# Kernel optimization log

Measured on AMD Instinct MI355X. Metric: run time of the kernel, lower is better.

The kernel has to match this reference:

```python
import jax, jax.numpy as jnp
import numpy as np

WIN = 7      # window_size (square)
HEADS = 6    # num_heads


def setup_inputs() -> dict:
    key = jax.random.key(0)
    k0, k1, k2, k3 = jax.random.split(key, 4)
    B, C, H, W = 8, 384, 56, 56
    x = jax.random.normal(k0, (B, C, H, W), jnp.float32)
    # 1x1 conv weights stored as (out, in) matrices
    w_qkv = jax.random.normal(k1, (3 * C, C), jnp.float32) * 0.02
    b_qkv = jnp.zeros((3 * C,), jnp.float32)
    w_proj = jax.random.normal(k2, (C, C), jnp.float32) * 0.02
    b_proj = jnp.zeros((C,), jnp.float32)
    bias_table = jax.random.normal(k3, (WIN * WIN, HEADS), jnp.float32) * 0.02
    return {"x": x, "w_qkv": w_qkv, "b_qkv": b_qkv, "w_proj": w_proj,
            "b_proj": b_proj, "bias_table": bias_table}


def reference(x, w_qkv, b_qkv, w_proj, b_proj, bias_table):
    B, C, H, W = x.shape
    heads, win = HEADS, WIN
    dph = C // heads
    scale = dph ** -0.5
    # qkv 1x1 conv -> (B, 3C, H, W)
    qkv = jnp.einsum('bcij,oc->boij', x, w_qkv) + b_qkv[None, :, None, None]
    q = qkv[:, :C] * scale
    k = qkv[:, C:2 * C]
    v = qkv[:, 2 * C:]
    p = win // 2
    kp = jnp.pad(k, ((0, 0), (0, 0), (p, p), (p, p)))  # (B,C,H+6,W+6)
    vp = jnp.pad(v, ((0, 0), (0, 0), (p, p), (p, p)))
    qh = q.reshape(B, heads, dph, H, W)
    # local window QK scores: fixed 49 shifted slices (no big patch tensor)
    scores = []
    for idx in range(win * win):
        dy, dx = idx // win, idx % win
        ks = kp[:, :, dy:dy + H, dx:dx + W].reshape(B, heads, dph, H, W)
        scores.append(jnp.einsum('bhdij,bhdij->bhij', qh, ks))
    attn = jnp.stack(scores, axis=2)  # (B, heads, 49, H, W)
    # forward() adds relative_position_bias * 0 (faithful no-op)
    attn = attn + bias_table.T.reshape(1, heads, win * win, 1, 1) * 0.0
    attn = jax.nn.softmax(attn, axis=2)
    # apply attention to V via the same 49 shifted slices
    out = jnp.zeros((B, heads, dph, H, W), x.dtype)
    for idx in range(win * win):
        dy, dx = idx // win, idx % win
        vs = vp[:, :, dy:dy + H, dx:dx + W].reshape(B, heads, dph, H, W)
        out = out + attn[:, :, idx][:, :, None] * vs
    out = out.reshape(B, C, H, W)
    # proj 1x1 conv; proj_drop has p=0.0 -> identity
    out = jnp.einsum('bcij,oc->boij', out, w_proj) + b_proj[None, :, None, None]
    return out
```

## Files before the change

kernel.cpp:

```cpp
#include <hip/hip_runtime.h>
#include <hip/hip_bf16.h>
#include <stdint.h>

#define HWsz 3136
#define Hh   56
#define Cc   384
#define NHEADS 6
#define NB   8

typedef __attribute__((ext_vector_type(8))) short short8;
typedef __attribute__((ext_vector_type(4))) short short4v;
typedef __attribute__((ext_vector_type(4))) float f32x4;

static __device__ __forceinline__ short f2bf(float f) {
  __hip_bfloat16 h = __float2bfloat16(f);
  return (short)__builtin_bit_cast(unsigned short, h);
}
static __device__ __forceinline__ void gload16(const void* g, void* l) {
  __builtin_amdgcn_global_load_lds(
      (const __attribute__((address_space(1))) void*)g,
      (__attribute__((address_space(3))) void*)l, 16, 0, 0);
}

__global__ void prep_weights(const float* __restrict__ wq, const float* __restrict__ wp,
                             short* __restrict__ wqt, short* __restrict__ wpt) {
  int stride = gridDim.x * blockDim.x;
  for (int i = blockIdx.x * blockDim.x + threadIdx.x; i < 3 * Cc * Cc; i += stride) {
    int o = i / Cc, k = i - o * Cc;
    float v = wq[i] * (o < Cc ? 0.125f : 1.0f);
    wqt[(((o >> 7) * 12 + (k >> 5)) * 128 + (o & 127)) * 40 + (k & 31)] = f2bf(v);
  }
  for (int i = blockIdx.x * blockDim.x + threadIdx.x; i < Cc * Cc; i += stride) {
    int o = i / Cc, k = i - o * Cc;
    wpt[(((o >> 7) * 12 + (k >> 5)) * 128 + (o & 127)) * 40 + (k & 31)] = f2bf(wp[i]);
  }
}

__global__ __launch_bounds__(256) void transpose_x(const float* __restrict__ x,
                                                   short* __restrict__ xTt) {
  __shared__ float tf[32][129];
  const int blk = blockIdx.x;
  const int b = blk & 7;
  const int idx = blk >> 3;
  const int pni = idx >> 2;
  const int kg  = idx & 3;
  const int p0 = pni * 128;
  const int t = threadIdx.x;
  const float* xb = x + (size_t)b * Cc * HWsz;
  short* outb = xTt + ((size_t)(b * 25 + pni)) * 12 * 5120;
  const int cc = t >> 3, pq = t & 7;
  const int orow = t >> 1, ohf = t & 1;
  for (int k0 = kg * 3; k0 < kg * 3 + 3; ++k0) {
    const float* crow = xb + (size_t)(k0 * 32 + cc) * HWsz;
#pragma unroll
    for (int i = 0; i < 4; ++i) {
      int p = p0 + pq * 16 + i * 4;
      if (p > HWsz - 4) p = HWsz - 4;
      f32x4 v = *(const f32x4*)(crow + p);
      tf[cc][pq * 16 + i * 4 + 0] = v[0];
      tf[cc][pq * 16 + i * 4 + 1] = v[1];
      tf[cc][pq * 16 + i * 4 + 2] = v[2];
      tf[cc][pq * 16 + i * 4 + 3] = v[3];
    }
    __syncthreads();
    short8 s0, s1;
#pragma unroll
    for (int i = 0; i < 8; ++i) s0[i] = f2bf(tf[ohf * 16 + i][orow]);
#pragma unroll
    for (int i = 0; i < 8; ++i) s1[i] = f2bf(tf[ohf * 16 + 8 + i][orow]);
    short* orp = outb + k0 * 5120 + orow * 40 + ohf * 16;
    *(short8*)(orp)     = s0;
    *(short8*)(orp + 8) = s1;
    __syncthreads();
  }
}

template<int MODE>
__global__ __launch_bounds__(256) void gemm_bf16(
    const short* __restrict__ At, const short* __restrict__ Bt,
    const float* __restrict__ bias, void* __restrict__ o1, void* __restrict__ o2)
{
  constexpr int NOM = (MODE == 0 ? 9 : 3);
  const int b   = blockIdx.x & 7;
  const int idx = blockIdx.x >> 3;
  const int omi = idx % NOM;
  const int pni = idx / NOM;
  const int om0 = omi * 128, pn0 = pni * 128;
  __shared__ short lA[5120];
  __shared__ short lB[5120];
  const int t = threadIdx.x, lane = t & 63, wave = t >> 6;
  const int wm = (wave >> 1) * 64, wn = (wave & 1) * 64;
  const int fr = lane & 15, fo = lane >> 4;
  f32x4 acc[4][4] = {};
  const short* Abase = At + omi * 12 * 5120;
  const short* Bbase = Bt + ((size_t)(b * 25 + pni)) * 12 * 5120;

  for (int k0i = 0; k0i < 12; ++k0i) {
    __syncthreads();
    const short* Ats = Abase + k0i * 5120;
    const short* Bts = Bbase + k0i * 5120;
#pragma unroll
    for (int c = 0; c < 5; ++c) {
      const int g = wave * 5 + c;
      const short* src = (g < 10 ? Ats + g * 512 : Bts + (g - 10) * 512) + lane * 8;
      short* dst = (g < 10 ? lA + g * 512 : lB + (g - 10) * 512);
      gload16(src, dst);
    }
    __syncthreads();
    short8 af[4], bfr[4];
#pragma unroll
    for (int m = 0; m < 4; ++m) af[m]  = *(const short8*)(lA + (wm + m * 16 + fr) * 40 + fo * 8);
#pragma unroll
    for (int n = 0; n < 4; ++n) bfr[n] = *(const short8*)(lB + (wn + n * 16 + fr) * 40 + fo * 8);
#pragma unroll
    for (int m = 0; m < 4; ++m)
#pragma unroll
      for (int n = 0; n < 4; ++n)
        acc[m][n] = __builtin_amdgcn_mfma_f32_16x16x32_bf16(af[m], bfr[n], acc[m][n], 0, 0, 0);
  }
  if (MODE == 0) {
    if (om0 < 768) {
      short* outq = (short*)o1 + (size_t)b * HWsz * 768;
#pragma unroll
      for (int m = 0; m < 4; ++m) {
        int ob = om0 + wm + m * 16 + (lane >> 4) * 4;
        float bs[4];
#pragma unroll
        for (int r = 0; r < 4; ++r) { int o = ob + r; bs[r] = bias[o] * (o < Cc ? 0.125f : 1.0f); }
#pragma unroll
        for (int n = 0; n < 4; ++n) {
          int p = pn0 + wn + n * 16 + fr;
          if (p < HWsz) {
            short4v s;
#pragma unroll
            for (int r = 0; r < 4; ++r) s[r] = f2bf(acc[m][n][r] + bs[r]);
            *(short4v*)(outq + (size_t)p * 768 + ob) = s;
          }
        }
      }
    } else {
      short* vtp = (short*)o2;
#pragma unroll
      for (int m = 0; m < 4; ++m) {
        int ob = om0 + wm + m * 16 + (lane >> 4) * 4;
#pragma unroll
        for (int n = 0; n < 4; ++n) {
          int p = pn0 + wn + n * 16 + fr;
          if (p < HWsz) {
            int ii = p / Hh, jj = p % Hh;
#pragma unroll
            for (int r = 0; r < 4; ++r) {
              int ch = ob + r - 768;
              vtp[((b * Cc + ch) * 62 + ii + 3) * 64 + jj + 3] = f2bf(acc[m][n][r] + bias[ob + r]);
            }
          }
        }
      }
    }
  } else {
    float* outo = (float*)o1 + (size_t)b * Cc * HWsz;
#pragma unroll
    for (int m = 0; m < 4; ++m) {
      int ob = om0 + wm + m * 16 + (lane >> 4) * 4;
#pragma unroll
      for (int n = 0; n < 4; ++n) {
        int p = pn0 + wn + n * 16 + fr;
        if (p < HWsz) {
#pragma unroll
          for (int r = 0; r < 4; ++r)
            outo[(size_t)(ob + r) * HWsz + p] = acc[m][n][r] + bias[ob + r];
        }
      }
    }
  }
}

__global__ __launch_bounds__(256) void attn_mfma(
    const short* __restrict__ qkv,
    const short* __restrict__ vtp,
    short* __restrict__ aoutT)
{
  __shared__ short P[64 * 40];
  const int blk = blockIdx.x;
  const int b = blk & 7;
  const int r_ = blk >> 3;
  const int h = r_ / 49;
  const int tile = r_ % 49;
  const int i0 = (tile / 7) * 8, j0 = (tile % 7) * 8;
  const int t = threadIdx.x, lane = t & 63, w = t >> 6;
  const int fr = lane & 15, fo = lane >> 4;

  const int q_idx = w * 16 + fr;
  const int qr = q_idx >> 3, qc = q_idx & 7;
  const int qkvb = b * HWsz * 768;

  const short* qp = qkv + qkvb + ((i0 + qr) * Hh + j0 + qc) * 768 + h * 64 + fo * 8;
  short8 qf0 = *(const short8*)(qp);
  short8 qf1 = *(const short8*)(qp + 32);

  const int kj = j0 + fr - 3;
  const bool jok = (unsigned)kj < (unsigned)Hh;
  const int kjs = kj < 0 ? 0 : (kj > Hh - 1 ? Hh - 1 : kj);
  const short* kcol = qkv + qkvb + Cc + h * 64 + fo * 8;

  const short8 z = (short8)0;
  f32x4 oacc[4] = {};
  float sum = 0.f;

#pragma unroll 2
  for (int kc = 0; kc < 7; ++kc) {
    short8 kf[2][2];
#pragma unroll
    for (int mloc = 0; mloc < 2; ++mloc) {
      int ki = i0 + 2 * kc + mloc - 3;
      bool ok = jok && ((unsigned)ki < (unsigned)Hh);
      int kis = ki < 0 ? 0 : (ki > Hh - 1 ? Hh - 1 : ki);
      const short8* ka = (const short8*)(kcol + (kis * Hh + kjs) * 768);
      short8 k0 = ka[0], k1 = ka[4];
      kf[mloc][0] = ok ? k0 : z;
      kf[mloc][1] = ok ? k1 : z;
    }
    short8 vf[4];
    const int vrow = i0 + 2 * kc + (fo >> 1);
    const int vcol = j0 + (fo & 1) * 8;
#pragma unroll
    for (int n = 0; n < 4; ++n)
      vf[n] = *(const short8*)(vtp + ((b * Cc + h * 64 + 16 * n + fr) * 62 + vrow) * 64 + vcol);
    f32x4 s0 = {}, s1 = {};
    s0 = __builtin_amdgcn_mfma_f32_16x16x32_bf16(kf[0][0], qf0, s0, 0, 0, 0);
    s0 = __builtin_amdgcn_mfma_f32_16x16x32_bf16(kf[0][1], qf1, s0, 0, 0, 0);
    s1 = __builtin_amdgcn_mfma_f32_16x16x32_bf16(kf[1][0], qf0, s1, 0, 0, 0);
    s1 = __builtin_amdgcn_mfma_f32_16x16x32_bf16(kf[1][1], qf1, s1, 0, 0, 0);
#pragma unroll
    for (int mloc = 0; mloc < 2; ++mloc) {
      const f32x4 sv = mloc ? s1 : s0;
      int dpr = 2 * kc + mloc - qr;
      bool rok = (unsigned)dpr <= 6u;
      short4v pk;
#pragma unroll
      for (int r = 0; r < 4; ++r) {
        int dpc = fo * 4 + r - qc;
        float e = (rok && (unsigned)dpc <= 6u) ? __expf(sv[r]) : 0.f;
        sum += e;
        pk[r] = f2bf(e);
      }
      *(short4v*)(P + q_idx * 40 + mloc * 16 + fo * 4) = pk;
    }
    short8 pa = *(const short8*)(P + q_idx * 40 + fo * 8);
#pragma unroll
    for (int n = 0; n < 4; ++n)
      oacc[n] = __builtin_amdgcn_mfma_f32_16x16x32_bf16(pa, vf[n], oacc[n], 0, 0, 0);
  }

  sum += __shfl_xor(sum, 16);
  sum += __shfl_xor(sum, 32);
  float inv[4];
#pragma unroll
  for (int r = 0; r < 4; ++r) inv[r] = 1.0f / __shfl(sum, fo * 4 + r);
  const int owr = i0 + 2 * w + (fo >> 1);
  const int owc = j0 + (fo & 1) * 4;
  short* ab = aoutT + (size_t)b * 25 * 12 * 5120;
#pragma unroll
  for (int n = 0; n < 4; ++n) {
    const int k0 = 2 * h + (n >> 1);
    const int kk = 16 * (n & 1) + fr;
#pragma unroll
    for (int r = 0; r < 4; ++r) {
      int p = owr * Hh + owc + r;
      ab[((size_t)((p >> 7) * 12 + k0)) * 5120 + (p & 127) * 40 + kk] = f2bf(oacc[n][r] * inv[r]);
    }
  }
}

extern "C" void kernel_launch(void* const* d_in, const int* in_sizes, int n_in,
                              void* d_out, int out_size, void* d_ws, size_t ws_size,
                              hipStream_t stream) {
  const float* x      = (const float*)d_in[0];
  const float* w_qkv  = (const float*)d_in[1];
  const float* b_qkv  = (const float*)d_in[2];
  const float* w_proj = (const float*)d_in[3];
  const float* b_proj = (const float*)d_in[4];

  char* ws = (char*)d_ws;
  short* qk  = (short*)ws;
  short* vtp = (short*)(ws + 38535168);
  short* xTt = (short*)(ws + 38535168 + 24379392);
  short* wqt = (short*)(ws + 38535168 + 24379392 + 24576000);
  short* wpt = (short*)(ws + 38535168 + 24379392 + 24576000 + 1105920);

  prep_weights<<<512, 256, 0, stream>>>(w_qkv, w_proj, wqt, wpt);
  hipMemsetAsync(vtp, 0, 24379392, stream);
  transpose_x<<<8 * 100, 256, 0, stream>>>(x, xTt);
  gemm_bf16<0><<<8 * 225, 256, 0, stream>>>(wqt, xTt, b_qkv, qk, vtp);
  attn_mfma<<<8 * 294, 256, 0, stream>>>(qk, vtp, xTt);
  gemm_bf16<1><<<8 * 75, 256, 0, stream>>>(wpt, xTt, b_proj, d_out, nullptr);
}
```

Baseline: 236.8 us.

## Process two tiles per attention block with K prefetch and MFMA priority

```diff
diff --git a/kernel.cpp b/kernel.cpp
--- a/kernel.cpp
+++ b/kernel.cpp
@@ -175,7 +175,7 @@
   }
 }
 
-__global__ __launch_bounds__(256) void attn_mfma(
+__global__ __launch_bounds__(256, 5) void attn_mfma(
     const short* __restrict__ qkv,
     const short* __restrict__ vtp,
     short* __restrict__ aoutT)
@@ -183,91 +183,109 @@
   __shared__ short P[64 * 40];
   const int blk = blockIdx.x;
   const int b = blk & 7;
-  const int r_ = blk >> 3;
-  const int h = r_ / 49;
-  const int tile = r_ % 49;
-  const int i0 = (tile / 7) * 8, j0 = (tile % 7) * 8;
+  const int rr = blk >> 3;
   const int t = threadIdx.x, lane = t & 63, w = t >> 6;
   const int fr = lane & 15, fo = lane >> 4;
-
-  const int q_idx = w * 16 + fr;
-  const int qr = q_idx >> 3, qc = q_idx & 7;
   const int qkvb = b * HWsz * 768;
-
-  const short* qp = qkv + qkvb + ((i0 + qr) * Hh + j0 + qc) * 768 + h * 64 + fo * 8;
-  short8 qf0 = *(const short8*)(qp);
-  short8 qf1 = *(const short8*)(qp + 32);
-
-  const int kj = j0 + fr - 3;
-  const bool jok = (unsigned)kj < (unsigned)Hh;
-  const int kjs = kj < 0 ? 0 : (kj > Hh - 1 ? Hh - 1 : kj);
-  const short* kcol = qkv + qkvb + Cc + h * 64 + fo * 8;
-
   const short8 z = (short8)0;
-  f32x4 oacc[4] = {};
-  float sum = 0.f;
-
-#pragma unroll 2
-  for (int kc = 0; kc < 7; ++kc) {
-    short8 kf[2][2];
-#pragma unroll
-    for (int mloc = 0; mloc < 2; ++mloc) {
-      int ki = i0 + 2 * kc + mloc - 3;
-      bool ok = jok && ((unsigned)ki < (unsigned)Hh);
-      int kis = ki < 0 ? 0 : (ki > Hh - 1 ? Hh - 1 : ki);
-      const short8* ka = (const short8*)(kcol + (kis * Hh + kjs) * 768);
-      short8 k0 = ka[0], k1 = ka[4];
-      kf[mloc][0] = ok ? k0 : z;
-      kf[mloc][1] = ok ? k1 : z;
-    }
-    short8 vf[4];
-    const int vrow = i0 + 2 * kc + (fo >> 1);
-    const int vcol = j0 + (fo & 1) * 8;
-#pragma unroll
-    for (int n = 0; n < 4; ++n)
-      vf[n] = *(const short8*)(vtp + ((b * Cc + h * 64 + 16 * n + fr) * 62 + vrow) * 64 + vcol);
-    f32x4 s0 = {}, s1 = {};
-    s0 = __builtin_amdgcn_mfma_f32_16x16x32_bf16(kf[0][0], qf0, s0, 0, 0, 0);
-    s0 = __builtin_amdgcn_mfma_f32_16x16x32_bf16(kf[0][1], qf1, s0, 0, 0, 0);
-    s1 = __builtin_amdgcn_mfma_f32_16x16x32_bf16(kf[1][0], qf0, s1, 0, 0, 0);
-    s1 = __builtin_amdgcn_mfma_f32_16x16x32_bf16(kf[1][1], qf1, s1, 0, 0, 0);
-#pragma unroll
-    for (int mloc = 0; mloc < 2; ++mloc) {
-      const f32x4 sv = mloc ? s1 : s0;
-      int dpr = 2 * kc + mloc - qr;
-      bool rok = (unsigned)dpr <= 6u;
-      short4v pk;
+  short* ab = aoutT + (size_t)b * 25 * 12 * 5120;
+
+#pragma unroll 1
+  for (int ti = 0; ti < 2; ++ti) {
+    const int tau = rr * 2 + ti;
+    const int h = tau / 49, tile = tau % 49;
+    const int i0 = (tile / 7) * 8, j0 = (tile % 7) * 8;
+
+    const int q_idx = w * 16 + fr;
+    const int qr = q_idx >> 3, qc = q_idx & 7;
+    const short* qp = qkv + qkvb + ((i0 + qr) * Hh + j0 + qc) * 768 + h * 64 + fo * 8;
+    short8 qf0 = *(const short8*)(qp);
+    short8 qf1 = *(const short8*)(qp + 32);
+
+    const int kj = j0 + fr - 3;
+    const bool jok = (unsigned)kj < (unsigned)Hh;
+    const int kjs = kj < 0 ? 0 : (kj > Hh - 1 ? Hh - 1 : kj);
+    const short* kcol = qkv + qkvb + Cc + h * 64 + fo * 8;
+
+    f32x4 oacc[4] = {};
+    float sum = 0.f;
+
+    short8 kf00, kf01, kf10, kf11;
+    {
+      int ki0 = i0 - 3;      int kis0 = ki0 < 0 ? 0 : (ki0 > Hh - 1 ? Hh - 1 : ki0);
+      int ki1 = i0 - 2;      int kis1 = ki1 < 0 ? 0 : (ki1 > Hh - 1 ? Hh - 1 : ki1);
+      const short8* ka = (const short8*)(kcol + (kis0 * Hh + kjs) * 768);
+      const short8* kb = (const short8*)(kcol + (kis1 * Hh + kjs) * 768);
+      kf00 = ka[0]; kf01 = ka[4]; kf10 = kb[0]; kf11 = kb[4];
+    }
+
+#pragma unroll
+    for (int kc = 0; kc < 7; ++kc) {
+      short8 vf[4];
+      const int vrow = i0 + 2 * kc + (fo >> 1);
+      const int vcol = j0 + (fo & 1) * 8;
+#pragma unroll
+      for (int n = 0; n < 4; ++n)
+        vf[n] = *(const short8*)(vtp + ((b * Cc + h * 64 + 16 * n + fr) * 62 + vrow) * 64 + vcol);
+      short8 nf00 = z, nf01 = z, nf10 = z, nf11 = z;
+      if (kc < 6) {
+        int ki0 = i0 + 2 * kc - 1;  int kis0 = ki0 < 0 ? 0 : (ki0 > Hh - 1 ? Hh - 1 : ki0);
+        int ki1 = i0 + 2 * kc;      int kis1 = ki1 < 0 ? 0 : (ki1 > Hh - 1 ? Hh - 1 : ki1);
+        const short8* ka = (const short8*)(kcol + (kis0 * Hh + kjs) * 768);
+        const short8* kb = (const short8*)(kcol + (kis1 * Hh + kjs) * 768);
+        nf00 = ka[0]; nf01 = ka[4]; nf10 = kb[0]; nf11 = kb[4];
+      }
+      const bool ok0 = jok && ((unsigned)(i0 + 2 * kc - 3) < (unsigned)Hh);
+      const bool ok1 = jok && ((unsigned)(i0 + 2 * kc - 2) < (unsigned)Hh);
+      short8 a00 = ok0 ? kf00 : z, a01 = ok0 ? kf01 : z;
+      short8 a10 = ok1 ? kf10 : z, a11 = ok1 ? kf11 : z;
+      f32x4 s0 = {}, s1 = {};
+      __builtin_amdgcn_s_setprio(1);
+      s0 = __builtin_amdgcn_mfma_f32_16x16x32_bf16(a00, qf0, s0, 0, 0, 0);
+      s0 = __builtin_amdgcn_mfma_f32_16x16x32_bf16(a01, qf1, s0, 0, 0, 0);
+      s1 = __builtin_amdgcn_mfma_f32_16x16x32_bf16(a10, qf0, s1, 0, 0, 0);
+      s1 = __builtin_amdgcn_mfma_f32_16x16x32_bf16(a11, qf1, s1, 0, 0, 0);
+      __builtin_amdgcn_s_setprio(0);
+#pragma unroll
+      for (int mloc = 0; mloc < 2; ++mloc) {
+        const f32x4 sv = mloc ? s1 : s0;
+        int dpr = 2 * kc + mloc - qr;
+        bool rok = (unsigned)dpr <= 6u;
+        short4v pk;
+#pragma unroll
+        for (int r = 0; r < 4; ++r) {
+          int dpc = fo * 4 + r - qc;
+          float e = (rok && (unsigned)dpc <= 6u) ? __expf(sv[r]) : 0.f;
+          sum += e;
+          pk[r] = f2bf(e);
+        }
+        *(short4v*)(P + q_idx * 40 + mloc * 16 + fo * 4) = pk;
+      }
+      short8 pa = *(const short8*)(P + q_idx * 40 + fo * 8);
+      __builtin_amdgcn_s_setprio(1);
+#pragma unroll
+      for (int n = 0; n < 4; ++n)
+        oacc[n] = __builtin_amdgcn_mfma_f32_16x16x32_bf16(pa, vf[n], oacc[n], 0, 0, 0);
+      __builtin_amdgcn_s_setprio(0);
+      if (kc < 6) { kf00 = nf00; kf01 = nf01; kf10 = nf10; kf11 = nf11; }
+    }
+
+    sum += __shfl_xor(sum, 16);
+    sum += __shfl_xor(sum, 32);
+    float inv[4];
+#pragma unroll
+    for (int r = 0; r < 4; ++r) inv[r] = 1.0f / __shfl(sum, fo * 4 + r);
+    const int owr = i0 + 2 * w + (fo >> 1);
+    const int owc = j0 + (fo & 1) * 4;
+#pragma unroll
+    for (int n = 0; n < 4; ++n) {
+      const int k0 = 2 * h + (n >> 1);
+      const int kk = 16 * (n & 1) + fr;
 #pragma unroll
       for (int r = 0; r < 4; ++r) {
-        int dpc = fo * 4 + r - qc;
-        float e = (rok && (unsigned)dpc <= 6u) ? __expf(sv[r]) : 0.f;
-        sum += e;
-        pk[r] = f2bf(e);
-      }
-      *(short4v*)(P + q_idx * 40 + mloc * 16 + fo * 4) = pk;
-    }
-    short8 pa = *(const short8*)(P + q_idx * 40 + fo * 8);
-#pragma unroll
-    for (int n = 0; n < 4; ++n)
-      oacc[n] = __builtin_amdgcn_mfma_f32_16x16x32_bf16(pa, vf[n], oacc[n], 0, 0, 0);
-  }
-
-  sum += __shfl_xor(sum, 16);
-  sum += __shfl_xor(sum, 32);
-  float inv[4];
-#pragma unroll
-  for (int r = 0; r < 4; ++r) inv[r] = 1.0f / __shfl(sum, fo * 4 + r);
-  const int owr = i0 + 2 * w + (fo >> 1);
-  const int owc = j0 + (fo & 1) * 4;
-  short* ab = aoutT + (size_t)b * 25 * 12 * 5120;
-#pragma unroll
-  for (int n = 0; n < 4; ++n) {
-    const int k0 = 2 * h + (n >> 1);
-    const int kk = 16 * (n & 1) + fr;
-#pragma unroll
-    for (int r = 0; r < 4; ++r) {
-      int p = owr * Hh + owc + r;
-      ab[((size_t)((p >> 7) * 12 + k0)) * 5120 + (p & 127) * 40 + kk] = f2bf(oacc[n][r] * inv[r]);
+        int p = owr * Hh + owc + r;
+        ab[((size_t)((p >> 7) * 12 + k0)) * 5120 + (p & 127) * 40 + kk] = f2bf(oacc[n][r] * inv[r]);
+      }
     }
   }
 }
@@ -292,6 +310,6 @@
   hipMemsetAsync(vtp, 0, 24379392, stream);
   transpose_x<<<8 * 100, 256, 0, stream>>>(x, xTt);
   gemm_bf16<0><<<8 * 225, 256, 0, stream>>>(wqt, xTt, b_qkv, qk, vtp);
-  attn_mfma<<<8 * 294, 256, 0, stream>>>(qk, vtp, xTt);
+  attn_mfma<<<8 * 147, 256, 0, stream>>>(qk, vtp, xTt);
   gemm_bf16<1><<<8 * 75, 256, 0, stream>>>(wpt, xTt, b_proj, d_out, nullptr);
 }
```

Result: slower. 244.7 us (+3.3%).

## Stage K and V halo tiles in LDS with zero-padded K image

Applied to the files above, without the earlier changes.

```diff
diff --git a/kernel.cpp b/kernel.cpp
--- a/kernel.cpp
+++ b/kernel.cpp
@@ -78,7 +78,8 @@
 template<int MODE>
 __global__ __launch_bounds__(256) void gemm_bf16(
     const short* __restrict__ At, const short* __restrict__ Bt,
-    const float* __restrict__ bias, void* __restrict__ o1, void* __restrict__ o2)
+    const float* __restrict__ bias, void* __restrict__ o1, void* __restrict__ o2,
+    void* __restrict__ o3)
 {
   constexpr int NOM = (MODE == 0 ? 9 : 3);
   const int b   = blockIdx.x & 7;
@@ -119,14 +120,14 @@
         acc[m][n] = __builtin_amdgcn_mfma_f32_16x16x32_bf16(af[m], bfr[n], acc[m][n], 0, 0, 0);
   }
   if (MODE == 0) {
-    if (om0 < 768) {
-      short* outq = (short*)o1 + (size_t)b * HWsz * 768;
+    if (om0 < 384) {
+      short* outq = (short*)o1 + (size_t)b * HWsz * 384;
 #pragma unroll
       for (int m = 0; m < 4; ++m) {
         int ob = om0 + wm + m * 16 + (lane >> 4) * 4;
         float bs[4];
 #pragma unroll
-        for (int r = 0; r < 4; ++r) { int o = ob + r; bs[r] = bias[o] * (o < Cc ? 0.125f : 1.0f); }
+        for (int r = 0; r < 4; ++r) bs[r] = bias[ob + r] * 0.125f;
 #pragma unroll
         for (int n = 0; n < 4; ++n) {
           int p = pn0 + wn + n * 16 + fr;
@@ -134,12 +135,29 @@
             short4v s;
 #pragma unroll
             for (int r = 0; r < 4; ++r) s[r] = f2bf(acc[m][n][r] + bs[r]);
-            *(short4v*)(outq + (size_t)p * 768 + ob) = s;
+            *(short4v*)(outq + (size_t)p * 384 + ob) = s;
           }
         }
       }
+    } else if (om0 < 768) {
+      short* kimg = (short*)o2;
+#pragma unroll
+      for (int m = 0; m < 4; ++m) {
+        int ob = om0 + wm + m * 16 + (lane >> 4) * 4;
+#pragma unroll
+        for (int n = 0; n < 4; ++n) {
+          int p = pn0 + wn + n * 16 + fr;
+          if (p < HWsz) {
+            int ii = p / Hh, jj = p % Hh;
+            short4v s;
+#pragma unroll
+            for (int r = 0; r < 4; ++r) s[r] = f2bf(acc[m][n][r] + bias[ob + r]);
+            *(short4v*)(kimg + ((size_t)(b * 62 + ii + 3) * 64 + jj + 3) * 384 + ob - 384) = s;
+          }
+        }
+      }
     } else {
-      short* vtp = (short*)o2;
+      short* vtp = (short*)o3;
 #pragma unroll
       for (int m = 0; m < 4; ++m) {
         int ob = om0 + wm + m * 16 + (lane >> 4) * 4;
@@ -176,10 +194,13 @@
 }
 
 __global__ __launch_bounds__(256) void attn_mfma(
-    const short* __restrict__ qkv,
+    const short* __restrict__ qbuf,
+    const short* __restrict__ kimg,
     const short* __restrict__ vtp,
     short* __restrict__ aoutT)
 {
+  __shared__ short Kl[224 * 64];
+  __shared__ short Vl[64 * 232];
   __shared__ short P[64 * 40];
   const int blk = blockIdx.x;
   const int b = blk & 7;
@@ -190,47 +211,50 @@
   const int t = threadIdx.x, lane = t & 63, w = t >> 6;
   const int fr = lane & 15, fo = lane >> 4;
 
+  {
+    const short* kb = kimg + ((size_t)(b * 62 + i0) * 64 + j0) * 384 + h * 64;
+#pragma unroll
+    for (int it = 0; it < 7; ++it) {
+      int tau = it * 256 + t;
+      int pos = tau >> 3, c = tau & 7;
+      int prow = pos >> 4, pcol = pos & 15;
+      short8 v = *(const short8*)(kb + ((size_t)prow * 64 + pcol) * 384 + c * 8);
+      *(short8*)(Kl + pos * 64 + ((c ^ (pos & 7)) * 8)) = v;
+    }
+    const short* vb = vtp + ((size_t)(b * Cc + h * 64) * 62 + i0) * 64 + j0;
+#pragma unroll
+    for (int it = 0; it < 7; ++it) {
+      int tau = it * 256 + t;
+      int ch = tau / 28, rp = tau - ch * 28;
+      int row = rp >> 1, half = rp & 1;
+      short8 v = *(const short8*)(vb + ((size_t)ch * 62 + row) * 64 + half * 8);
+      *(short8*)(Vl + ch * 232 + row * 16 + half * 8) = v;
+    }
+  }
+
   const int q_idx = w * 16 + fr;
   const int qr = q_idx >> 3, qc = q_idx & 7;
-  const int qkvb = b * HWsz * 768;
-
-  const short* qp = qkv + qkvb + ((i0 + qr) * Hh + j0 + qc) * 768 + h * 64 + fo * 8;
+  const short* qp = qbuf + ((size_t)(b * HWsz) + (i0 + qr) * Hh + j0 + qc) * 384 + h * 64 + fo * 8;
   short8 qf0 = *(const short8*)(qp);
   short8 qf1 = *(const short8*)(qp + 32);
 
-  const int kj = j0 + fr - 3;
-  const bool jok = (unsigned)kj < (unsigned)Hh;
-  const int kjs = kj < 0 ? 0 : (kj > Hh - 1 ? Hh - 1 : kj);
-  const short* kcol = qkv + qkvb + Cc + h * 64 + fo * 8;
-
-  const short8 z = (short8)0;
+  __syncthreads();
+
   f32x4 oacc[4] = {};
   float sum = 0.f;
 
-#pragma unroll 2
+#pragma unroll
   for (int kc = 0; kc < 7; ++kc) {
-    short8 kf[2][2];
-#pragma unroll
-    for (int mloc = 0; mloc < 2; ++mloc) {
-      int ki = i0 + 2 * kc + mloc - 3;
-      bool ok = jok && ((unsigned)ki < (unsigned)Hh);
-      int kis = ki < 0 ? 0 : (ki > Hh - 1 ? Hh - 1 : ki);
-      const short8* ka = (const short8*)(kcol + (kis * Hh + kjs) * 768);
-      short8 k0 = ka[0], k1 = ka[4];
-      kf[mloc][0] = ok ? k0 : z;
-      kf[mloc][1] = ok ? k1 : z;
-    }
-    short8 vf[4];
-    const int vrow = i0 + 2 * kc + (fo >> 1);
-    const int vcol = j0 + (fo & 1) * 8;
-#pragma unroll
-    for (int n = 0; n < 4; ++n)
-      vf[n] = *(const short8*)(vtp + ((b * Cc + h * 64 + 16 * n + fr) * 62 + vrow) * 64 + vcol);
+    const int pos0 = 32 * kc + fr, pos1 = pos0 + 16;
+    short8 a00 = *(const short8*)(Kl + pos0 * 64 + ((fo       ^ (pos0 & 7)) * 8));
+    short8 a01 = *(const short8*)(Kl + pos0 * 64 + (((4 + fo) ^ (pos0 & 7)) * 8));
+    short8 a10 = *(const short8*)(Kl + pos1 * 64 + ((fo       ^ (pos1 & 7)) * 8));
+    short8 a11 = *(const short8*)(Kl + pos1 * 64 + (((4 + fo) ^ (pos1 & 7)) * 8));
     f32x4 s0 = {}, s1 = {};
-    s0 = __builtin_amdgcn_mfma_f32_16x16x32_bf16(kf[0][0], qf0, s0, 0, 0, 0);
-    s0 = __builtin_amdgcn_mfma_f32_16x16x32_bf16(kf[0][1], qf1, s0, 0, 0, 0);
-    s1 = __builtin_amdgcn_mfma_f32_16x16x32_bf16(kf[1][0], qf0, s1, 0, 0, 0);
-    s1 = __builtin_amdgcn_mfma_f32_16x16x32_bf16(kf[1][1], qf1, s1, 0, 0, 0);
+    s0 = __builtin_amdgcn_mfma_f32_16x16x32_bf16(a00, qf0, s0, 0, 0, 0);
+    s0 = __builtin_amdgcn_mfma_f32_16x16x32_bf16(a01, qf1, s0, 0, 0, 0);
+    s1 = __builtin_amdgcn_mfma_f32_16x16x32_bf16(a10, qf0, s1, 0, 0, 0);
+    s1 = __builtin_amdgcn_mfma_f32_16x16x32_bf16(a11, qf1, s1, 0, 0, 0);
 #pragma unroll
     for (int mloc = 0; mloc < 2; ++mloc) {
       const f32x4 sv = mloc ? s1 : s0;
@@ -248,8 +272,10 @@
     }
     short8 pa = *(const short8*)(P + q_idx * 40 + fo * 8);
 #pragma unroll
-    for (int n = 0; n < 4; ++n)
-      oacc[n] = __builtin_amdgcn_mfma_f32_16x16x32_bf16(pa, vf[n], oacc[n], 0, 0, 0);
+    for (int n = 0; n < 4; ++n) {
+      short8 vf = *(const short8*)(Vl + (n * 16 + fr) * 232 + kc * 32 + fo * 8);
+      oacc[n] = __builtin_amdgcn_mfma_f32_16x16x32_bf16(pa, vf, oacc[n], 0, 0, 0);
+    }
   }
 
   sum += __shfl_xor(sum, 16);
@@ -282,16 +308,17 @@
   const float* b_proj = (const float*)d_in[4];
 
   char* ws = (char*)d_ws;
-  short* qk  = (short*)ws;
-  short* vtp = (short*)(ws + 38535168);
-  short* xTt = (short*)(ws + 38535168 + 24379392);
-  short* wqt = (short*)(ws + 38535168 + 24379392 + 24576000);
-  short* wpt = (short*)(ws + 38535168 + 24379392 + 24576000 + 1105920);
+  short* qbuf = (short*)ws;
+  short* kimg = (short*)(ws + 19267584);
+  short* vtp  = (short*)(ws + 19267584 + 24379392);
+  short* xTt  = (short*)(ws + 19267584 + 24379392 + 24379392);
+  short* wqt  = (short*)(ws + 19267584 + 24379392 + 24379392 + 24576000);
+  short* wpt  = (short*)(ws + 19267584 + 24379392 + 24379392 + 24576000 + 1105920);
 
   prep_weights<<<512, 256, 0, stream>>>(w_qkv, w_proj, wqt, wpt);
-  hipMemsetAsync(vtp, 0, 24379392, stream);
+  hipMemsetAsync(kimg, 0, 24379392u + 24379392u, stream);
   transpose_x<<<8 * 100, 256, 0, stream>>>(x, xTt);
-  gemm_bf16<0><<<8 * 225, 256, 0, stream>>>(wqt, xTt, b_qkv, qk, vtp);
-  attn_mfma<<<8 * 294, 256, 0, stream>>>(qk, vtp, xTt);
-  gemm_bf16<1><<<8 * 75, 256, 0, stream>>>(wpt, xTt, b_proj, d_out, nullptr);
-}
+  gemm_bf16<0><<<8 * 225, 256, 0, stream>>>(wqt, xTt, b_qkv, qbuf, kimg, vtp);
+  attn_mfma<<<8 * 294, 256, 0, stream>>>(qbuf, kimg, vtp, xTt);
+  gemm_bf16<1><<<8 * 75, 256, 0, stream>>>(wpt, xTt, b_proj, d_out, nullptr, nullptr);
+}
```

New measurement: 207.7 us. 1.14x faster.
